# Kernel tuning notes

Measured on AMD Instinct MI355X. Metric: run time of the kernel, lower is better.

The kernel has to match this reference:

```python
import jax, jax.numpy as jnp
import numpy as np

DIM = 256        # word / relation / entity-type embedding dim
STATEDIM = 256   # agent state dim
VOCAB = 100000
REL_COUNT = 25
T = 128          # sentence length


def _lstm(wvs, Wih, Whh, bih, bhh, reverse):
    # PyTorch LSTMCell gate order: i, f, g, o
    def step(carry, x):
        h, c = carry
        g = x @ Wih.T + bih + h @ Whh.T + bhh
        i, f, gg, o = jnp.split(g, 4)
        c = jax.nn.sigmoid(f) * c + jax.nn.sigmoid(i) * jnp.tanh(gg)
        h = jax.nn.sigmoid(o) * jnp.tanh(c)
        return (h, c), h
    init = (jnp.zeros((DIM,), jnp.float32), jnp.zeros((DIM,), jnp.float32))
    _, hs = jax.lax.scan(step, init, wvs, reverse=reverse)
    return hs


def setup_inputs() -> dict:
    key = jax.random.key(0)
    ks = jax.random.split(key, 32)
    def p(i, shape, scale=0.05):
        return (jax.random.normal(ks[i], shape) * scale).astype(jnp.float32)
    return {
        "text": jax.random.randint(ks[0], (T,), 0, VOCAB, dtype=jnp.int32),
        "wordvector": p(1, (VOCAB, DIM)),
        "relvec": p(2, (REL_COUNT + 1, DIM)),
        "entvec": p(3, (7, DIM)),
        "WihL": p(4, (4 * DIM, DIM)), "WhhL": p(5, (4 * DIM, DIM)),
        "bihL": p(6, (4 * DIM,)), "bhhL": p(7, (4 * DIM,)),
        "WihR": p(8, (4 * DIM, DIM)), "WhhR": p(9, (4 * DIM, DIM)),
        "bihR": p(10, (4 * DIM,)), "bhhR": p(11, (4 * DIM,)),
        "Wt": p(12, (STATEDIM, 3 * DIM + STATEDIM)), "bt": p(13, (STATEDIM,)),
        "Wp": p(14, (REL_COUNT + 1, STATEDIM)), "bp": p(15, (REL_COUNT + 1,)),
        "Wb": p(16, (STATEDIM, 3 * DIM + 2 * STATEDIM)), "bb": p(17, (STATEDIM,)),
        "Wpl": p(18, (REL_COUNT, 7, STATEDIM)), "bpl": p(19, (REL_COUNT, 7)),
        "Wtt": p(20, (STATEDIM, STATEDIM)), "btt": p(21, (STATEDIM,)),
        "Wtb": p(22, (STATEDIM, STATEDIM)), "btb": p(23, (STATEDIM,)),
        "Wbt": p(24, (STATEDIM, STATEDIM)), "bbt": p(25, (STATEDIM,)),
    }


def reference(text, wordvector, relvec, entvec, WihL, WhhL, bihL, bhhL,
              WihR, WhhR, bihR, bhhR, Wt, bt, Wp, bp, Wb, bb, Wpl, bpl,
              Wtt, btt, Wtb, btb, Wbt, bbt):
    # mode = "test_NER": deterministic argmax sampling, dropout disabled.
    wvs = wordvector[text]                               # [T, DIM]
    front = _lstm(wvs, WihL, WhhL, bihL, bhhL, False)    # [T, DIM]
    back = _lstm(wvs, WihR, WhhR, bihR, bhhR, True)      # [T, DIM]
    wordin = jnp.concatenate([front, back], axis=1)      # [T, 2*DIM]

    def bot_rollout(rel_idx, target, memb0):
        Wr, br = Wpl[rel_idx], bpl[rel_idx]              # per-relation head
        def stepb(carry, w):
            memb, ab = carry
            inpb = jnp.concatenate([w, entvec[ab], memb, target])
            outb = jnp.tanh(inpb @ Wb.T + bb)            # dropout off (test)
            probb = jax.nn.softmax(outb @ Wr.T + br)
            ab2 = jnp.argmax(probb).astype(jnp.int32)
            return (outb, ab2), (ab2, probb[ab2])
        (membf, _), (acts, aps) = jax.lax.scan(
            stepb, (memb0, jnp.zeros((), jnp.int32)), wordin)
        return membf, acts, aps

    def top_step(carry, w):
        mem, rel_action = carry
        inp = jnp.concatenate([w, relvec[rel_action], mem])
        outp = jnp.tanh(inp @ Wt.T + bt)                 # dropout off (test)
        prob = jax.nn.softmax(outp @ Wp.T + bp)
        action = jnp.argmax(prob).astype(jnp.int32)
        actprob = prob[action]
        do_ner = action > 0
        rel_next = jnp.where(do_ner, action, rel_action)
        rel_idx = jnp.maximum(action, 1) - 1
        target = outp @ Wtt.T + btt
        memb0 = outp @ Wtb.T + btb
        membf, acts, aps = bot_rollout(rel_idx, target, memb0)
        mem_after = membf @ Wbt.T + bbt
        mem_next = jnp.where(do_ner, mem_after, outp)
        acts = jnp.where(do_ner, acts, 0)
        aps = jnp.where(do_ner, aps, 0.0)
        return (mem_next, rel_next), (action, actprob, acts, aps)

    init = (jnp.zeros((STATEDIM,), jnp.float32), jnp.zeros((), jnp.int32))
    _, (top_actions, top_actprobs, bot_actions, bot_actprobs) = jax.lax.scan(
        top_step, init, wordin)
    # bot rows where no NER sub-rollout fired are zero-filled (orig: empty lists)
    return top_actions, top_actprobs, bot_actions, bot_actprobs
```

## Files before the change

kernel.cpp:

```cpp
#include <hip/hip_runtime.h>
#include <float.h>

constexpr int SEQ  = 128;
constexpr int D    = 256;
constexpr int G    = 1024;
constexpr int NREL = 26;
constexpr int NENT = 7;

typedef float v2f __attribute__((ext_vector_type(2)));
typedef float v4f __attribute__((ext_vector_type(4)));

__global__ void k_trans(const float* __restrict__ in, float* __restrict__ out,
                        int rows, int cols, int in_stride, int in_off)
{
    int idx = blockIdx.x * 256 + threadIdx.x;
    if (idx >= rows * cols) return;
    int i = idx % rows;
    int k = idx / rows;
    out[idx] = in[(size_t)i * in_stride + in_off + k];
}

__global__ __launch_bounds__(1024) void k_xg(
    const int* __restrict__ text, const float* __restrict__ wv,
    const float* __restrict__ Wih, const float* __restrict__ bih,
    const float* __restrict__ bhh, float* __restrict__ xg)
{
    int t = blockIdx.x, j = threadIdx.x;
    const float* x  = wv + (size_t)text[t] * D;
    const float* wr = Wih + (size_t)j * D;
    float acc = bih[j] + bhh[j];
    for (int k = 0; k < D; ++k) acc += x[k] * wr[k];
    xg[t * G + j] = acc;
}

__global__ __launch_bounds__(1024) void k_lstm(
    const float* __restrict__ xgF, const float* __restrict__ xgB,
    const float* __restrict__ WHTF, const float* __restrict__ WHTB,
    float* __restrict__ wordin)
{
    int dir = blockIdx.x;
    const float* xg  = dir ? xgB  : xgF;
    const float* WHT = dir ? WHTB : WHTF;
    __shared__ float h[D], c[D], g[G];
    int j = threadIdx.x;
    if (j < D) { h[j] = 0.f; c[j] = 0.f; }
    __syncthreads();
    for (int s = 0; s < SEQ; ++s) {
        int t = dir ? (SEQ - 1 - s) : s;
        float acc = xg[t * G + j];
        for (int k = 0; k < D; ++k) acc += WHT[k * G + j] * h[k];
        g[j] = acc;
        __syncthreads();
        if (j < D) {
            float si = 1.f / (1.f + expf(-g[j]));
            float sf = 1.f / (1.f + expf(-g[D + j]));
            float gg = tanhf(g[2 * D + j]);
            float so = 1.f / (1.f + expf(-g[3 * D + j]));
            float cn = sf * c[j] + si * gg;
            float hn = so * tanhf(cn);
            c[j] = cn; h[j] = hn;
            wordin[t * (2 * D) + dir * D + j] = hn;
        }
        __syncthreads();
    }
}

__global__ __launch_bounds__(256) void k_prep2(
    const float* __restrict__ wordin,
    const float* __restrict__ WTWT, const float* __restrict__ WBWT,
    const float* __restrict__ WTRT, const float* __restrict__ WBET,
    const float* __restrict__ relvec, const float* __restrict__ entvec,
    const float* __restrict__ btv, const float* __restrict__ bbv,
    float* __restrict__ TW, float* __restrict__ BW,
    float* __restrict__ RV, float* __restrict__ EV)
{
    int b = blockIdx.x, i = threadIdx.x;
    if (b < SEQ) {
        const float* w = wordin + b * (2 * D);
        float a1 = btv[i], a2 = bbv[i];
        for (int j = 0; j < 2 * D; ++j) {
            float wv = w[j];
            a1 += wv * WTWT[j * D + i];
            a2 += wv * WBWT[j * D + i];
        }
        TW[b * D + i] = a1;
        BW[b * D + i] = a2;
    } else if (b < SEQ + NREL) {
        int r = b - SEQ;
        const float* x = relvec + r * D;
        float a = 0.f;
        for (int k = 0; k < D; ++k) a += x[k] * WTRT[k * D + i];
        RV[r * D + i] = a;
    } else {
        int e = b - SEQ - NREL;
        const float* x = entvec + e * D;
        float a = 0.f;
        for (int k = 0; k < D; ++k) a += x[k] * WBET[k * D + i];
        EV[e * D + i] = a;
    }
}

__global__ __launch_bounds__(256) void k_m1(
    const float* __restrict__ WBGT, const float* __restrict__ Wtt,
    float* __restrict__ M1T)
{
    int j = blockIdx.x, i = threadIdx.x;
    float a = 0.f;
    for (int k = 0; k < D; ++k) a = fmaf(WBGT[k * D + i], Wtt[k * D + j], a);
    M1T[j * D + i] = a;
}

__global__ __launch_bounds__(256) void k_c1(
    const float* __restrict__ WBGT, const float* __restrict__ btt,
    float* __restrict__ c1)
{
    int i = threadIdx.x;
    float a = 0.f;
    for (int k = 0; k < D; ++k) a = fmaf(WBGT[k * D + i], btt[k], a);
    c1[i] = a;
}

__global__ __launch_bounds__(256) void k_packBg(
    const float* __restrict__ Wb, float* __restrict__ WGL)
{
    int f = blockIdx.x * 256 + threadIdx.x;
    if (f >= 512 * 56) return;
    int f4 = f >> 2, c = f & 3;
    int tid = f4 & 511, n = f4 >> 9;
    int h = tid >> 8, i = tid & 255;
    WGL[f] = Wb[(size_t)i * (5 * D) + 3 * D + h * 128 + 4 * n + c];
}

__global__ __launch_bounds__(256) void k_packBl(
    const float* __restrict__ Wb, float* __restrict__ WLDS)
{
    int f = blockIdx.x * 256 + threadIdx.x;
    if (f >= 512 * 72) return;
    int f4 = f >> 2, c = f & 3;
    int l = f4 & 63, rest = f4 >> 6;
    int j = rest % 18, w = rest / 18;
    int tid = w * 64 + l;
    int h = tid >> 8, i = tid & 255;
    WLDS[f] = Wb[(size_t)i * (5 * D) + 3 * D + h * 128 + 56 + 4 * j + c];
}

__device__ inline float mv_half(const float* __restrict__ Wcol,
                                const float* __restrict__ x)
{
    float a0 = 0.f, a1 = 0.f, a2 = 0.f, a3 = 0.f;
    #pragma unroll 8
    for (int kk = 0; kk < 128; kk += 4) {
        a0 = fmaf(Wcol[(kk + 0) * D], x[kk + 0], a0);
        a1 = fmaf(Wcol[(kk + 1) * D], x[kk + 1], a1);
        a2 = fmaf(Wcol[(kk + 2) * D], x[kk + 2], a2);
        a3 = fmaf(Wcol[(kk + 3) * D], x[kk + 3], a3);
    }
    return (a0 + a1) + (a2 + a3);
}

template<int W>
__device__ inline void grp_smax(float lv, int n, int lane, int& am, float& pm)
{
    float mx = lv;
    #pragma unroll
    for (int off = W / 2; off; off >>= 1) mx = fmaxf(mx, __shfl_xor(mx, off));
    float e  = (lane < n) ? expf(lv - mx) : 0.f;
    float se = e;
    #pragma unroll
    for (int off = W / 2; off; off >>= 1) se += __shfl_xor(se, off);
    float p  = (lane < n) ? (e / se) : -1.f;
    float q  = p;
    #pragma unroll
    for (int off = W / 2; off; off >>= 1) q = fmaxf(q, __shfl_xor(q, off));
    unsigned long long mask = __ballot(p == q);
    am = __ffsll((long long)mask) - 1;
    pm = q;
}

#define FMA_AB(Wv, Xv)                                                        \
    { v4f xx_ = (Xv);                                                         \
      A0 = __builtin_elementwise_fma((v2f){(Wv).x, (Wv).y},                   \
                                     (v2f){xx_.x, xx_.y}, A0);                \
      A1 = __builtin_elementwise_fma((v2f){(Wv).z, (Wv).w},                   \
                                     (v2f){xx_.z, xx_.w}, A1); }
#define FMA_CD(Wv, Xv)                                                        \
    { v4f xx_ = (Xv);                                                         \
      A2 = __builtin_elementwise_fma((v2f){(Wv).x, (Wv).y},                   \
                                     (v2f){xx_.x, xx_.y}, A2);                \
      A3 = __builtin_elementwise_fma((v2f){(Wv).z, (Wv).w},                   \
                                     (v2f){xx_.z, xx_.w}, A3); }

#define LC(j0)                                                                \
    { v4f la = wbase[(j0 + 0) * 64], lb = wbase[(j0 + 1) * 64],               \
          lc = wbase[(j0 + 2) * 64], ld = wbase[(j0 + 3) * 64];               \
      FMA_AB(la, xb[14 + j0 + 0]) FMA_CD(lb, xb[14 + j0 + 1])                 \
      FMA_AB(lc, xb[14 + j0 + 2]) FMA_CD(ld, xb[14 + j0 + 3])                 \
      __builtin_amdgcn_sched_barrier(0); }

__global__ __launch_bounds__(512)
void k_mainB(
    const float* __restrict__ TW,   const float* __restrict__ BW,
    const float* __restrict__ RV,   const float* __restrict__ EV,
    const float* __restrict__ WTMT, const float* __restrict__ WTBT,
    const float* __restrict__ WBTT, const float* __restrict__ M1T,
    const float* __restrict__ c1v,  const float* __restrict__ WLDS,
    const float* __restrict__ WGL,
    const float* __restrict__ Wp,   const float* __restrict__ bp,
    const float* __restrict__ Wpl,  const float* __restrict__ bpl,
    const float* __restrict__ btb,  const float* __restrict__ bbt,
    float* __restrict__ out)
{
    const int tid  = threadIdx.x;
    const int lane = tid & 63;
    const int wv8  = tid >> 6;
    const int lwv  = wv8 & 3;
    const int h    = tid >> 8;
    const int i    = tid & 255;
    const bool lower = (tid < 256);

    __shared__ __align__(16) float wlds[512 * 72];
    __shared__ __align__(16) float xbuf[2][D];
    __shared__ __align__(16) float psA[2][D];
    __shared__ __align__(16) float mem[D], outv[D];
    __shared__ __align__(16) float WrSh[NENT * D];
    __shared__ float lpart[4][32];
    __shared__ float brSh[8];

    {
        const float4* g4 = reinterpret_cast<const float4*>(WLDS);
        float4* w4 = reinterpret_cast<float4*>(wlds);
        #pragma unroll
        for (int it = 0; it < 18; ++it) w4[tid + it * 512] = g4[tid + it * 512];
    }
    if (lower) mem[i] = 0.f;
    __syncthreads();

    const v4f* wbase =
        reinterpret_cast<const v4f*>(wlds) + (size_t)wv8 * (18 * 64) + lane;
    const v4f* gl = reinterpret_cast<const v4f*>(WGL) + tid;

    const float* WTMh = WTMT + (size_t)h * 128 * D + i;
    const float* WTBh = WTBT + (size_t)h * 128 * D + i;
    const float* WBTh = WBTT + (size_t)h * 128 * D + i;
    const float* M1h  = M1T  + (size_t)h * 128 * D + i;

    int rel = 0;

    #pragma unroll 1
    for (int t = 0; t < SEQ; ++t) {
        psA[h][i] = mv_half(WTMh, mem + h * 128);
        __syncthreads();
        if (lower) {
            float tot = psA[0][i] + psA[1][i] +
                        TW[t * D + i] + RV[rel * D + i];
            float outp = tanhf(tot);
            outv[i] = outp;
            #pragma unroll 2
            for (int r = 0; r < NREL; ++r) {
                float pp = outp * Wp[r * D + i];
                #pragma unroll
                for (int off = 32; off; off >>= 1) pp += __shfl_xor(pp, off);
                if (lane == 0) lpart[lwv][r] = pp;
            }
        }
        __syncthreads();
        float lv = -FLT_MAX;
        if (lane < NREL)
            lv = lpart[0][lane] + lpart[1][lane] + lpart[2][lane] +
                 lpart[3][lane] + bp[lane];
        int am; float pm;
        grp_smax<32>(lv, NREL, lane, am, pm);
        if (tid == 0) { out[t] = (float)am; out[SEQ + t] = pm; }
        const int action = am;

        if (action > 0) {
            rel = action;
            psA[h][i] = mv_half(WTBh, outv + h * 128);
            const size_t wb0 = (size_t)(action - 1) * NENT * D;
            for (int k = tid; k < NENT * D; k += 512) WrSh[k] = Wpl[wb0 + k];
            if (tid < NENT) brSh[tid] = bpl[(action - 1) * NENT + tid];
            __syncthreads();
            if (lower) xbuf[0][i] = psA[0][i] + psA[1][i] + btb[i];
            __syncthreads();
            psA[h][i] = mv_half(M1h, outv + h * 128);
            __syncthreads();
            float btm = 0.f, bwc = 0.f, evn = 0.f;
            if (lower) {
                btm = psA[0][i] + psA[1][i] + c1v[i];
                bwc = BW[i];
                evn = EV[i];
            }
            __syncthreads();

            int p = 0, ab = 0;
            #pragma unroll 1
            for (int s = 0; s < SEQ; ++s) {
                const v4f* glv = gl;
                asm volatile("" : "+v"(glv));
                v4f g0  = glv[0 * 512],  g1  = glv[1 * 512],
                    g2  = glv[2 * 512],  g3  = glv[3 * 512],
                    g4  = glv[4 * 512],  g5  = glv[5 * 512],
                    g6  = glv[6 * 512],  g7  = glv[7 * 512],
                    g8  = glv[8 * 512],  g9  = glv[9 * 512],
                    g10 = glv[10 * 512], g11 = glv[11 * 512],
                    g12 = glv[12 * 512], g13 = glv[13 * 512];
                __builtin_amdgcn_sched_barrier(0);

                const v4f* xb = reinterpret_cast<const v4f*>(xbuf[p] + h * 128);
                v2f A0 = {0.f, 0.f}, A1 = {0.f, 0.f},
                    A2 = {0.f, 0.f}, A3 = {0.f, 0.f};
                LC(0) LC(4) LC(8) LC(12)
                { v4f la = wbase[16 * 64], lb = wbase[17 * 64];
                  FMA_AB(la, xb[30]) FMA_CD(lb, xb[31]) }
                __builtin_amdgcn_sched_barrier(0);
                FMA_AB(g0,  xb[0])  FMA_CD(g1,  xb[1])
                FMA_AB(g2,  xb[2])  FMA_CD(g3,  xb[3])
                __builtin_amdgcn_sched_barrier(0);
                FMA_AB(g4,  xb[4])  FMA_CD(g5,  xb[5])
                FMA_AB(g6,  xb[6])  FMA_CD(g7,  xb[7])
                __builtin_amdgcn_sched_barrier(0);
                FMA_AB(g8,  xb[8])  FMA_CD(g9,  xb[9])
                FMA_AB(g10, xb[10]) FMA_CD(g11, xb[11])
                __builtin_amdgcn_sched_barrier(0);
                FMA_AB(g12, xb[12]) FMA_CD(g13, xb[13])
                v2f AS = (A0 + A1) + (A2 + A3);
                float ms = AS.x + AS.y;
                psA[h][i] = ms;
                __syncthreads();
                if (lower) {
                    float tot = ms + psA[1][i] + bwc + evn + btm;
                    float ob = tanhf(tot);
                    xbuf[p ^ 1][i] = ob;
                    #pragma unroll
                    for (int r = 0; r < NENT; ++r) {
                        float pp = ob * WrSh[r * D + i];
                        #pragma unroll
                        for (int off = 32; off; off >>= 1)
                            pp += __shfl_xor(pp, off);
                        if (lane == 0) lpart[lwv][r] = pp;
                    }
                }
                __syncthreads();
                float lv2 = -FLT_MAX;
                if (lane < NENT)
                    lv2 = lpart[0][lane] + lpart[1][lane] + lpart[2][lane] +
                          lpart[3][lane] + brSh[lane];
                int am2; float pm2;
                grp_smax<8>(lv2, NENT, lane, am2, pm2);
                if (tid == 0) {
                    out[2 * SEQ + t * SEQ + s] = (float)am2;
                    out[2 * SEQ + SEQ * SEQ + t * SEQ + s] = pm2;
                }
                ab = am2;
                if (lower) {
                    int sn = (s + 1 < SEQ) ? s + 1 : s;
                    bwc = BW[sn * D + i];
                    evn = EV[ab * D + i];
                }
                p ^= 1;
            }
            psA[h][i] = mv_half(WBTh, xbuf[p] + h * 128);
            __syncthreads();
            if (lower) mem[i] = psA[0][i] + psA[1][i] + bbt[i];
            __syncthreads();
        } else {
            if (lower) mem[i] = outv[i];
            if (tid < SEQ) {
                out[2 * SEQ + t * SEQ + tid] = 0.f;
                out[2 * SEQ + SEQ * SEQ + t * SEQ + tid] = 0.f;
            }
            __syncthreads();
        }
    }
}

extern "C" void kernel_launch(void* const* d_in, const int* in_sizes, int n_in,
                              void* d_out, int out_size, void* d_ws, size_t ws_size,
                              hipStream_t stream)
{
    (void)in_sizes; (void)n_in; (void)out_size; (void)ws_size;
    const int*   text       = (const int*)  d_in[0];
    const float* wordvector = (const float*)d_in[1];
    const float* relvec     = (const float*)d_in[2];
    const float* entvec     = (const float*)d_in[3];
    const float* WihL = (const float*)d_in[4];  const float* WhhL = (const float*)d_in[5];
    const float* bihL = (const float*)d_in[6];  const float* bhhL = (const float*)d_in[7];
    const float* WihR = (const float*)d_in[8];  const float* WhhR = (const float*)d_in[9];
    const float* bihR = (const float*)d_in[10]; const float* bhhR = (const float*)d_in[11];
    const float* Wt   = (const float*)d_in[12]; const float* bt   = (const float*)d_in[13];
    const float* Wp   = (const float*)d_in[14]; const float* bp   = (const float*)d_in[15];
    const float* Wb   = (const float*)d_in[16]; const float* bb   = (const float*)d_in[17];
    const float* Wpl  = (const float*)d_in[18]; const float* bpl  = (const float*)d_in[19];
    const float* Wtt  = (const float*)d_in[20]; const float* btt  = (const float*)d_in[21];
    const float* Wtb  = (const float*)d_in[22]; const float* btb  = (const float*)d_in[23];
    const float* Wbt  = (const float*)d_in[24]; const float* bbt  = (const float*)d_in[25];

    float* ws = (float*)d_ws;
    size_t o = 0;
    auto take = [&](size_t n) { float* p = ws + o; o += n; return p; };
    float* XGF    = take(SEQ * G);
    float* XGB    = take(SEQ * G);
    float* WHLT   = take(D * G);
    float* WHRT   = take(D * G);
    float* WORDIN = take(SEQ * 2 * D);
    float* TW     = take(SEQ * D);
    float* BW     = take(SEQ * D);
    float* RVb    = take(NREL * D);
    float* EVb    = take(NENT * D);
    float* WTWT   = take(2 * D * D);
    float* WTRT   = take(D * D);
    float* WTMT   = take(D * D);
    float* WBWT   = take(2 * D * D);
    float* WBET   = take(D * D);
    float* WBGT   = take(D * D);
    float* WTBT   = take(D * D);
    float* WBTT   = take(D * D);
    float* M1T    = take(D * D);
    float* C1     = take(D);
    float* WLDS   = take(512 * 72);
    float* WGL    = take(512 * 56);

    auto tr = [&](const float* in, float* outp, int rows, int cols, int stride, int off) {
        int n = rows * cols;
        k_trans<<<(n + 255) / 256, 256, 0, stream>>>(in, outp, rows, cols, stride, off);
    };
    tr(WhhL, WHLT, G, D, D, 0);
    tr(WhhR, WHRT, G, D, D, 0);
    tr(Wt,  WTWT, D, 2 * D, G, 0);
    tr(Wt,  WTRT, D, D, G, 512);
    tr(Wt,  WTMT, D, D, G, 768);
    tr(Wb,  WBWT, D, 2 * D, 5 * D, 0);
    tr(Wb,  WBET, D, D, 5 * D, 512);
    tr(Wb,  WBGT, D, D, 5 * D, 1024);
    tr(Wtb, WTBT, D, D, D, 0);
    tr(Wbt, WBTT, D, D, D, 0);

    k_m1<<<D, D, 0, stream>>>(WBGT, Wtt, M1T);
    k_c1<<<1, D, 0, stream>>>(WBGT, btt, C1);
    k_packBl<<<(512 * 72 + 255) / 256, 256, 0, stream>>>(Wb, WLDS);
    k_packBg<<<(512 * 56 + 255) / 256, 256, 0, stream>>>(Wb, WGL);

    k_xg<<<SEQ, 1024, 0, stream>>>(text, wordvector, WihL, bihL, bhhL, XGF);
    k_xg<<<SEQ, 1024, 0, stream>>>(text, wordvector, WihR, bihR, bhhR, XGB);
    k_lstm<<<2, 1024, 0, stream>>>(XGF, XGB, WHLT, WHRT, WORDIN);
    k_prep2<<<SEQ + NREL + NENT, 256, 0, stream>>>(WORDIN, WTWT, WBWT, WTRT, WBET,
                                                   relvec, entvec, bt, bb,
                                                   TW, BW, RVb, EVb);
    k_mainB<<<1, 512, 0, stream>>>(TW, BW, RVb, EVb, WTMT, WTBT, WBTT, M1T, C1,
                                   WLDS, WGL, Wp, bp, Wpl, bpl, btb, bbt,
                                   (float*)d_out);
}
```

Measured before the change: 63.10 ms.

## Pin bottom-LSTM weight slice in registers and prefetch global slice across steps

The bottom-rollout matvec weights are now split three ways. 32 columns per thread are packed to stay in VGPRs for the whole kernel, 72 stay in LDS, and the remaining 24 are streamed from global memory. The global part is prefetched for the next step right after its FMAs, so the load latency overlaps the barrier and softmax work. Barriers are replaced by a lighter one that waits only on LDS counters. The change raises register pressure, which could cause spills or reduce scheduling slack in this single-block serial kernel.

```diff
diff --git a/kernel.cpp b/kernel.cpp
--- a/kernel.cpp
+++ b/kernel.cpp
@@ -120,18 +120,28 @@
     c1[i] = a;
 }
 
-__global__ __launch_bounds__(256) void k_packBg(
+__global__ __launch_bounds__(256) void k_packCr(
+    const float* __restrict__ Wb, float* __restrict__ WREG)
+{
+    int e = blockIdx.x * 256 + threadIdx.x;
+    if (e >= 512 * 32) return;
+    int tid = e >> 5, q = e & 31;
+    int h = tid >> 8, i = tid & 255;
+    WREG[e] = Wb[(size_t)i * (5 * D) + 3 * D + h * 128 + q];
+}
+
+__global__ __launch_bounds__(256) void k_packCg(
     const float* __restrict__ Wb, float* __restrict__ WGL)
 {
     int f = blockIdx.x * 256 + threadIdx.x;
-    if (f >= 512 * 56) return;
+    if (f >= 512 * 24) return;
     int f4 = f >> 2, c = f & 3;
     int tid = f4 & 511, n = f4 >> 9;
     int h = tid >> 8, i = tid & 255;
-    WGL[f] = Wb[(size_t)i * (5 * D) + 3 * D + h * 128 + 4 * n + c];
-}
-
-__global__ __launch_bounds__(256) void k_packBl(
+    WGL[f] = Wb[(size_t)i * (5 * D) + 3 * D + h * 128 + 32 + 4 * n + c];
+}
+
+__global__ __launch_bounds__(256) void k_packCl(
     const float* __restrict__ Wb, float* __restrict__ WLDS)
 {
     int f = blockIdx.x * 256 + threadIdx.x;
@@ -197,14 +207,18 @@
       FMA_AB(lc, xb[14 + j0 + 2]) FMA_CD(ld, xb[14 + j0 + 3])                 \
       __builtin_amdgcn_sched_barrier(0); }
 
+#define BARX()                                                                \
+    do { asm volatile("s_waitcnt lgkmcnt(0)" ::: "memory");                   \
+         __builtin_amdgcn_s_barrier(); } while (0)
+
 __global__ __launch_bounds__(512)
-void k_mainB(
+void k_mainC(
     const float* __restrict__ TW,   const float* __restrict__ BW,
     const float* __restrict__ RV,   const float* __restrict__ EV,
     const float* __restrict__ WTMT, const float* __restrict__ WTBT,
     const float* __restrict__ WBTT, const float* __restrict__ M1T,
-    const float* __restrict__ c1v,  const float* __restrict__ WLDS,
-    const float* __restrict__ WGL,
+    const float* __restrict__ c1v,  const float* __restrict__ WREG,
+    const float* __restrict__ WLDS, const float* __restrict__ WGL,
     const float* __restrict__ Wp,   const float* __restrict__ bp,
     const float* __restrict__ Wpl,  const float* __restrict__ bpl,
     const float* __restrict__ btb,  const float* __restrict__ bbt,
@@ -227,12 +241,17 @@
     __shared__ float brSh[8];
 
     {
-        const float4* g4 = reinterpret_cast<const float4*>(WLDS);
+        const float4* g4s = reinterpret_cast<const float4*>(WLDS);
         float4* w4 = reinterpret_cast<float4*>(wlds);
         #pragma unroll
-        for (int it = 0; it < 18; ++it) w4[tid + it * 512] = g4[tid + it * 512];
+        for (int it = 0; it < 18; ++it) w4[tid + it * 512] = g4s[tid + it * 512];
     }
     if (lower) mem[i] = 0.f;
+
+    const v4f* r4 = reinterpret_cast<const v4f*>(WREG) + tid * 8;
+    v4f wr0 = r4[0], wr1 = r4[1], wr2 = r4[2], wr3 = r4[3];
+    v4f wr4 = r4[4], wr5 = r4[5], wr6 = r4[6], wr7 = r4[7];
+
     __syncthreads();
 
     const v4f* wbase =
@@ -292,20 +311,17 @@
             }
             __syncthreads();
 
+            v4f g0, g1, g2, g3, g4, g5;
+            {
+                const v4f* glv = gl;
+                asm volatile("" : "+v"(glv));
+                g0 = glv[0 * 512]; g1 = glv[1 * 512]; g2 = glv[2 * 512];
+                g3 = glv[3 * 512]; g4 = glv[4 * 512]; g5 = glv[5 * 512];
+            }
+
             int p = 0, ab = 0;
             #pragma unroll 1
             for (int s = 0; s < SEQ; ++s) {
-                const v4f* glv = gl;
-                asm volatile("" : "+v"(glv));
-                v4f g0  = glv[0 * 512],  g1  = glv[1 * 512],
-                    g2  = glv[2 * 512],  g3  = glv[3 * 512],
-                    g4  = glv[4 * 512],  g5  = glv[5 * 512],
-                    g6  = glv[6 * 512],  g7  = glv[7 * 512],
-                    g8  = glv[8 * 512],  g9  = glv[9 * 512],
-                    g10 = glv[10 * 512], g11 = glv[11 * 512],
-                    g12 = glv[12 * 512], g13 = glv[13 * 512];
-                __builtin_amdgcn_sched_barrier(0);
-
                 const v4f* xb = reinterpret_cast<const v4f*>(xbuf[p] + h * 128);
                 v2f A0 = {0.f, 0.f}, A1 = {0.f, 0.f},
                     A2 = {0.f, 0.f}, A3 = {0.f, 0.f};
@@ -313,20 +329,25 @@
                 { v4f la = wbase[16 * 64], lb = wbase[17 * 64];
                   FMA_AB(la, xb[30]) FMA_CD(lb, xb[31]) }
                 __builtin_amdgcn_sched_barrier(0);
-                FMA_AB(g0,  xb[0])  FMA_CD(g1,  xb[1])
-                FMA_AB(g2,  xb[2])  FMA_CD(g3,  xb[3])
+                FMA_AB(wr0, xb[0]) FMA_CD(wr1, xb[1])
+                FMA_AB(wr2, xb[2]) FMA_CD(wr3, xb[3])
                 __builtin_amdgcn_sched_barrier(0);
-                FMA_AB(g4,  xb[4])  FMA_CD(g5,  xb[5])
-                FMA_AB(g6,  xb[6])  FMA_CD(g7,  xb[7])
+                FMA_AB(wr4, xb[4]) FMA_CD(wr5, xb[5])
+                FMA_AB(wr6, xb[6]) FMA_CD(wr7, xb[7])
                 __builtin_amdgcn_sched_barrier(0);
-                FMA_AB(g8,  xb[8])  FMA_CD(g9,  xb[9])
-                FMA_AB(g10, xb[10]) FMA_CD(g11, xb[11])
-                __builtin_amdgcn_sched_barrier(0);
-                FMA_AB(g12, xb[12]) FMA_CD(g13, xb[13])
+                FMA_AB(g0, xb[8])  FMA_CD(g1, xb[9])
+                FMA_AB(g2, xb[10]) FMA_CD(g3, xb[11])
+                FMA_AB(g4, xb[12]) FMA_CD(g5, xb[13])
+                {
+                    const v4f* glv = gl;
+                    asm volatile("" : "+v"(glv));
+                    g0 = glv[0 * 512]; g1 = glv[1 * 512]; g2 = glv[2 * 512];
+                    g3 = glv[3 * 512]; g4 = glv[4 * 512]; g5 = glv[5 * 512];
+                }
                 v2f AS = (A0 + A1) + (A2 + A3);
                 float ms = AS.x + AS.y;
                 psA[h][i] = ms;
-                __syncthreads();
+                BARX();
                 if (lower) {
                     float tot = ms + psA[1][i] + bwc + evn + btm;
                     float ob = tanhf(tot);
@@ -340,7 +361,7 @@
                         if (lane == 0) lpart[lwv][r] = pp;
                     }
                 }
-                __syncthreads();
+                BARX();
                 float lv2 = -FLT_MAX;
                 if (lane < NENT)
                     lv2 = lpart[0][lane] + lpart[1][lane] + lpart[2][lane] +
@@ -417,8 +438,9 @@
     float* WBTT   = take(D * D);
     float* M1T    = take(D * D);
     float* C1     = take(D);
+    float* WREG   = take(512 * 32);
     float* WLDS   = take(512 * 72);
-    float* WGL    = take(512 * 56);
+    float* WGL    = take(512 * 24);
 
     auto tr = [&](const float* in, float* outp, int rows, int cols, int stride, int off) {
         int n = rows * cols;
@@ -437,8 +459,9 @@
 
     k_m1<<<D, D, 0, stream>>>(WBGT, Wtt, M1T);
     k_c1<<<1, D, 0, stream>>>(WBGT, btt, C1);
-    k_packBl<<<(512 * 72 + 255) / 256, 256, 0, stream>>>(Wb, WLDS);
-    k_packBg<<<(512 * 56 + 255) / 256, 256, 0, stream>>>(Wb, WGL);
+    k_packCr<<<(512 * 32 + 255) / 256, 256, 0, stream>>>(Wb, WREG);
+    k_packCl<<<(512 * 72 + 255) / 256, 256, 0, stream>>>(Wb, WLDS);
+    k_packCg<<<(512 * 24 + 255) / 256, 256, 0, stream>>>(Wb, WGL);
 
     k_xg<<<SEQ, 1024, 0, stream>>>(text, wordvector, WihL, bihL, bhhL, XGF);
     k_xg<<<SEQ, 1024, 0, stream>>>(text, wordvector, WihR, bihR, bhhR, XGB);
@@ -446,7 +469,7 @@
     k_prep2<<<SEQ + NREL + NENT, 256, 0, stream>>>(WORDIN, WTWT, WBWT, WTRT, WBET,
                                                    relvec, entvec, bt, bb,
                                                    TW, BW, RVb, EVb);
-    k_mainB<<<1, 512, 0, stream>>>(TW, BW, RVb, EVb, WTMT, WTBT, WBTT, M1T, C1,
-                                   WLDS, WGL, Wp, bp, Wpl, bpl, btb, bbt,
+    k_mainC<<<1, 512, 0, stream>>>(TW, BW, RVb, EVb, WTMT, WTBT, WBTT, M1T, C1,
+                                   WREG, WLDS, WGL, Wp, bp, Wpl, bpl, btb, bbt,
                                    (float*)d_out);
 }
```

Result: faster. 54.05 ms (-14.3%).
